# Optimization experiments

Hardware: AMD Instinct MI355X
Metric: run time of the kernel (lower is better)

Reference implementation:

```python
import jax, jax.numpy as jnp
import numpy as np

B, S, HID = 2, 2048, 2048
N_HEADS, N_KV = 16, 4
HEAD_DIM = HID // N_HEADS  # 128
N_REP = N_HEADS // N_KV
ROPE_THETA = 1000000.0


def setup_inputs() -> dict:
    key = jax.random.key(0)
    ks = jax.random.split(key, 8)
    s = 0.02
    # causal additive mask: 0 on/below diagonal, large negative above
    neg = jnp.finfo(jnp.float32).min
    causal = jnp.where(jnp.tril(jnp.ones((S, S), dtype=bool)), 0.0, neg)
    attention_mask = jnp.broadcast_to(causal[None, None], (B, 1, S, S)).astype(jnp.float32)
    return {
        "hidden_states": jax.random.normal(ks[0], (B, S, HID), jnp.float32),
        "Wq": jax.random.normal(ks[1], (HID, HID), jnp.float32) * s,
        "bq": jax.random.normal(ks[2], (HID,), jnp.float32) * s,
        "Wk": jax.random.normal(ks[3], (N_KV * HEAD_DIM, HID), jnp.float32) * s,
        "bk": jax.random.normal(ks[4], (N_KV * HEAD_DIM,), jnp.float32) * s,
        "Wv": jax.random.normal(ks[5], (N_KV * HEAD_DIM, HID), jnp.float32) * s,
        "bv": jax.random.normal(ks[6], (N_KV * HEAD_DIM,), jnp.float32) * s,
        "attention_mask": attention_mask,
        "position_ids": jnp.broadcast_to(jnp.arange(S, dtype=jnp.int64)[None], (B, S)),
    }


def _rotate_half(x):
    x1, x2 = jnp.split(x, 2, axis=-1)
    return jnp.concatenate((-x2, x1), axis=-1)


def _rope_cos_sin(position_ids, dtype):
    inv_freq = 1.0 / (ROPE_THETA ** (jnp.arange(0, HEAD_DIM, 2, dtype=jnp.float32) / HEAD_DIM))
    freqs = position_ids.astype(jnp.float32)[:, :, None] * inv_freq[None, None, :]  # [B,S,hd/2]
    emb = jnp.concatenate((freqs, freqs), axis=-1)  # [B,S,hd]
    return jnp.cos(emb).astype(dtype), jnp.sin(emb).astype(dtype)


def reference(hidden_states, Wq, bq, Wk, bk, Wv, bv, attention_mask, position_ids):
    b, s, _ = hidden_states.shape
    q = (hidden_states @ Wq.T + bq).reshape(b, s, N_HEADS, HEAD_DIM).transpose(0, 2, 1, 3)
    k = (hidden_states @ Wk.T + bk).reshape(b, s, N_KV, HEAD_DIM).transpose(0, 2, 1, 3)
    v = (hidden_states @ Wv.T + bv).reshape(b, s, N_KV, HEAD_DIM).transpose(0, 2, 1, 3)

    cos, sin = _rope_cos_sin(position_ids, hidden_states.dtype)
    cos, sin = cos[:, None], sin[:, None]  # unsqueeze head dim
    q = q * cos + _rotate_half(q) * sin
    k = k * cos + _rotate_half(k) * sin

    # GQA: repeat kv heads
    k = jnp.repeat(k, N_REP, axis=1)
    v = jnp.repeat(v, N_REP, axis=1)

    scores = jnp.einsum('bhqd,bhkd->bhqk', q, k) / jnp.sqrt(jnp.float32(HEAD_DIM)).astype(q.dtype)
    scores = scores + attention_mask
    probs = jax.nn.softmax(scores.astype(jnp.float32), axis=-1).astype(q.dtype)
    out = jnp.einsum('bhqk,bhkd->bhqd', probs, v)  # [B,H,S,hd]
    return out.transpose(0, 2, 1, 3).reshape(b, s, HID)
```

## Files before the change

### kernel.cpp

```cpp
#include <hip/hip_runtime.h>
#include <hip/hip_bf16.h>

typedef short bf16x8 __attribute__((ext_vector_type(8)));
typedef float f32x4 __attribute__((ext_vector_type(4)));
typedef unsigned int u32;
typedef unsigned short u16;

#define SLEN 2048
#define LOG2S 11

__device__ __forceinline__ u16 f2bf(float x) {
  u32 u = __builtin_bit_cast(u32, x);
  u = (u + 0x7fffu + ((u >> 16) & 1u)) >> 16;
  return (u16)u;
}

__device__ __forceinline__ void gload16(const void* g, void* l) {
  __builtin_amdgcn_global_load_lds((const __attribute__((address_space(1))) u32*)g,
                                   (__attribute__((address_space(3))) u32*)l, 16, 0, 0);
}

#define MFMA16(a, b, c) __builtin_amdgcn_mfma_f32_16x16x32_bf16((a), (b), (c), 0, 0, 0)

__global__ void k_convert(const float* __restrict__ src, u16* __restrict__ dst, int n4) {
  int i = blockIdx.x * blockDim.x + threadIdx.x;
  int stride = gridDim.x * blockDim.x;
  for (; i < n4; i += stride) {
    float4 v = reinterpret_cast<const float4*>(src)[i];
    ushort4 o;
    o.x = f2bf(v.x); o.y = f2bf(v.y); o.z = f2bf(v.z); o.w = f2bf(v.w);
    reinterpret_cast<ushort4*>(dst)[i] = o;
  }
}

__global__ void k_rope_table(float* __restrict__ ctab, float* __restrict__ stab) {
  int i = blockIdx.x * blockDim.x + threadIdx.x;
  int s = i >> 6, d = i & 63;
  float invf = powf(1.0e6f, -(float)d * (1.0f / 64.0f));
  float a = (float)s * invf;
  ctab[i] = cosf(a);
  stab[i] = sinf(a);
}

__global__ __launch_bounds__(256, 2) void k_proj(
    const u16* __restrict__ Xb, const u16* __restrict__ Wqb,
    const u16* __restrict__ Wkb, const u16* __restrict__ Wvb,
    const float* __restrict__ bq, const float* __restrict__ bk, const float* __restrict__ bv,
    const float* __restrict__ ctab, const float* __restrict__ stab,
    u16* __restrict__ Qb, u16* __restrict__ Kb, u16* __restrict__ Vt) {
  __shared__ __align__(16) char smb[65536];
  const int tid = threadIdx.x;
  const int lane = tid & 63;
  const int w = tid >> 6;
  const int l15 = lane & 15, g = lane >> 4;
  const int m0 = blockIdx.x * 128;
  const int y = blockIdx.y;
  int mode, head;
  const u16* W; const float* bias;
  if (y < 16)      { mode = 0; head = y;      W = Wqb; bias = bq; }
  else if (y < 20) { mode = 1; head = y - 16; W = Wkb; bias = bk; }
  else             { mode = 2; head = y - 20; W = Wvb; bias = bv; }
  const int n0 = head * 128;

  f32x4 acc[2][8] = {};

  const char* asrc[4]; const char* bsrc[4]; int ldo[4];
  #pragma unroll
  for (int it = 0; it < 4; ++it) {
    int c = it * 256 + tid;
    int row = c >> 3;
    int inner = ((c & 7) << 4) ^ ((row & 7) << 4);
    asrc[it] = (const char*)Xb + ((size_t)(m0 + row) * 2048) * 2 + inner;
    bsrc[it] = (const char*)W  + ((size_t)(n0 + row) * 2048) * 2 + inner;
    ldo[it] = c * 16;
  }

  auto STAGE = [&](int buf, int t) {
    char* ad = smb + buf * 16384;
    char* bd = smb + 32768 + buf * 16384;
    #pragma unroll
    for (int it = 0; it < 4; ++it) gload16(asrc[it] + t * 128, ad + ldo[it]);
    #pragma unroll
    for (int it = 0; it < 4; ++it) gload16(bsrc[it] + t * 128, bd + ldo[it]);
  };

  STAGE(0, 0);
  int cur = 0;
  for (int t = 0; t < 32; ++t) {
    if (t + 1 < 32) {
      STAGE(cur ^ 1, t + 1);
      asm volatile("s_waitcnt vmcnt(8)" ::: "memory");
    } else {
      asm volatile("s_waitcnt vmcnt(0)" ::: "memory");
    }
    __builtin_amdgcn_s_barrier();
    asm volatile("" ::: "memory");
    const char* Ac = smb + cur * 16384;
    const char* Bc = smb + 32768 + cur * 16384;
    #pragma unroll
    for (int kf = 0; kf < 2; ++kf) {
      const int innerk = kf * 64 + g * 16;
      const int rowA0 = w * 32 + l15;
      const int rowA1 = rowA0 + 16;
      bf16x8 a0 = *(const bf16x8*)(Ac + rowA0 * 128 + (innerk ^ ((rowA0 & 7) << 4)));
      bf16x8 a1 = *(const bf16x8*)(Ac + rowA1 * 128 + (innerk ^ ((rowA1 & 7) << 4)));
      #pragma unroll
      for (int j = 0; j < 8; ++j) {
        const int rowB = j * 16 + l15;
        bf16x8 bb = *(const bf16x8*)(Bc + rowB * 128 + (innerk ^ ((rowB & 7) << 4)));
        acc[0][j] = MFMA16(a0, bb, acc[0][j]);
        acc[1][j] = MFMA16(a1, bb, acc[1][j]);
      }
    }
    asm volatile("" ::: "memory");
    __builtin_amdgcn_s_barrier();
    cur ^= 1;
  }

  float biasv[8];
  #pragma unroll
  for (int j = 0; j < 8; ++j) biasv[j] = bias[n0 + j * 16 + l15];

  #pragma unroll
  for (int i = 0; i < 2; ++i) {
    #pragma unroll
    for (int r = 0; r < 4; ++r) {
      const int m = m0 + w * 32 + i * 16 + g * 4 + r;
      const int b = m >> LOG2S, s = m & (SLEN - 1);
      float v[8];
      #pragma unroll
      for (int j = 0; j < 8; ++j) v[j] = acc[i][j][r] + biasv[j];
      if (mode <= 1) {
        #pragma unroll
        for (int j = 0; j < 4; ++j) {
          const int f = j * 16 + l15;
          const float cv = ctab[s * 64 + f];
          const float sv = stab[s * 64 + f];
          const float lo = v[j], hi = v[j + 4];
          v[j]     = lo * cv - hi * sv;
          v[j + 4] = hi * cv + lo * sv;
        }
      }
      if (mode == 0) {
        u16* dst = Qb + (((size_t)(b * 16 + head) * SLEN + s) * 128);
        #pragma unroll
        for (int j = 0; j < 8; ++j) dst[j * 16 + l15] = f2bf(v[j]);
      } else if (mode == 1) {
        u16* dst = Kb + (((size_t)(b * 4 + head) * SLEN + s) * 128);
        #pragma unroll
        for (int j = 0; j < 8; ++j) dst[j * 16 + l15] = f2bf(v[j]);
      } else {
        const int sl = w * 32 + i * 16 + g * 4 + r;
        #pragma unroll
        for (int j = 0; j < 8; ++j) {
          const int d = j * 16 + l15;
          *(u16*)(smb + d * 256 + ((sl * 2) ^ ((d & 7) << 4))) = f2bf(v[j]);
        }
      }
    }
  }
  if (mode == 2) {
    __syncthreads();
    const int sbase = m0 & (SLEN - 1);
    const int bidx = m0 >> LOG2S;
    u16* Vg = Vt + ((size_t)(bidx * 4 + head) * 128) * SLEN;
    #pragma unroll
    for (int itr = 0; itr < 8; ++itr) {
      int c = itr * 256 + tid;
      int d = c >> 4, sc = c & 15;
      bf16x8 val = *(const bf16x8*)(smb + d * 256 + ((sc * 16) ^ ((d & 7) << 4)));
      *(bf16x8*)(Vg + (size_t)d * SLEN + sbase + sc * 8) = val;
    }
  }
}

__global__ __launch_bounds__(256, 2) void k_attn(
    const u16* __restrict__ Qb, const u16* __restrict__ Kb, const u16* __restrict__ Vt,
    float* __restrict__ Out) {
  __shared__ __align__(16) char smb[73728];
  const int tid = threadIdx.x, lane = tid & 63, w = tid >> 6;
  const int l15 = lane & 15, g = lane >> 4;
  const int qb_t = blockIdx.x;
  const int qa_t = 31 - qb_t;
  const int bh = blockIdx.y;
  const int b = bh >> 4, h = bh & 15, kv = h >> 2;
  const u16* Qbase = Qb + ((size_t)(b * 16 + h) * SLEN) * 128;
  const char* Kg = (const char*)(Kb + ((size_t)(b * 4 + kv) * SLEN) * 128);
  const char* Vg = (const char*)(Vt + ((size_t)(b * 4 + kv) * 128) * SLEN);
  char* Pw = smb + 65536 + w * 2048;

  const char* srcK[4]; const char* srcV[4]; int ldo[4];
  #pragma unroll
  for (int it = 0; it < 4; ++it) {
    int c = it * 256 + tid;
    ldo[it] = c * 16;
    int rk = c >> 4;
    srcK[it] = Kg + (size_t)rk * 256 + (((c & 15) << 4) ^ ((rk & 7) << 4));
    int rv = c >> 3;
    srcV[it] = Vg + (size_t)rv * 4096 + (((c & 7) << 4) ^ ((rv & 7) << 4));
  }

  const int qwa = qa_t * 64 + w * 16, qwb = qb_t * 64 + w * 16;
  bf16x8 qfa[4], qfb[4];
  #pragma unroll
  for (int kf = 0; kf < 4; ++kf) {
    qfa[kf] = *(const bf16x8*)(Qbase + (size_t)(qwa + l15) * 128 + kf * 32 + g * 8);
    qfb[kf] = *(const bf16x8*)(Qbase + (size_t)(qwb + l15) * 128 + kf * 32 + g * 8);
  }

  float ma[4], la[4], mb[4], lb[4];
  f32x4 oa[8] = {}, ob[8] = {};
  #pragma unroll
  for (int r = 0; r < 4; ++r) { ma[r] = mb[r] = -1e30f; la[r] = lb[r] = 0.f; }
  const float scale = 0.08838834764831845f;
  const int nt = qa_t + 1;

  auto STAGE = [&](int buf, int t) {
    char* kd = smb + buf * 16384;
    char* vd = smb + 32768 + buf * 16384;
    size_t ko = (size_t)t * 64;
    #pragma unroll
    for (int it = 0; it < 4; ++it) gload16(srcK[it] + ko * 256, kd + ldo[it]);
    #pragma unroll
    for (int it = 0; it < 4; ++it) gload16(srcV[it] + ko * 2, vd + ldo[it]);
  };

  STAGE(0, 0);
  int cur = 0;
  for (int t = 0; t < nt; ++t) {
    if (t + 1 < nt) {
      STAGE(cur ^ 1, t + 1);
      asm volatile("s_waitcnt vmcnt(8)" ::: "memory");
    } else {
      asm volatile("s_waitcnt vmcnt(0)" ::: "memory");
    }
    __builtin_amdgcn_s_barrier();
    asm volatile("" ::: "memory");
    const char* Kc = smb + cur * 16384;
    const char* Vc = smb + 32768 + cur * 16384;
    const int k0 = t * 64;

    auto softmax_pv = [&](f32x4* sac, float* mrun, float* lrun, f32x4* oacc,
                          int qw, bool diag) {
      float pr[4][4], alpha[4];
      #pragma unroll
      for (int r = 0; r < 4; ++r) {
        float sv[4];
        #pragma unroll
        for (int n = 0; n < 4; ++n) {
          float x = sac[n][r] * scale;
          if (diag) {
            int kvi = k0 + n * 16 + l15;
            int qi = qw + g * 4 + r;
            if (kvi > qi) x = -1e30f;
          }
          sv[n] = x;
        }
        float tm = fmaxf(fmaxf(sv[0], sv[1]), fmaxf(sv[2], sv[3]));
        tm = fmaxf(tm, __shfl_xor(tm, 1));
        tm = fmaxf(tm, __shfl_xor(tm, 2));
        tm = fmaxf(tm, __shfl_xor(tm, 4));
        tm = fmaxf(tm, __shfl_xor(tm, 8));
        float mnew = fmaxf(mrun[r], tm);
        alpha[r] = __expf(mrun[r] - mnew);
        mrun[r] = mnew;
        float ts = 0.f;
        #pragma unroll
        for (int n = 0; n < 4; ++n) { pr[n][r] = __expf(sv[n] - mnew); ts += pr[n][r]; }
        ts += __shfl_xor(ts, 1);
        ts += __shfl_xor(ts, 2);
        ts += __shfl_xor(ts, 4);
        ts += __shfl_xor(ts, 8);
        lrun[r] = lrun[r] * alpha[r] + ts;
      }
      #pragma unroll
      for (int nf = 0; nf < 8; ++nf) {
        #pragma unroll
        for (int r = 0; r < 4; ++r) oacc[nf][r] *= alpha[r];
      }
      #pragma unroll
      for (int n = 0; n < 4; ++n) {
        #pragma unroll
        for (int r = 0; r < 4; ++r) {
          const int row = g * 4 + r;
          const int colb = ((n * 16 + l15) * 2) ^ ((row & 7) << 4);
          *(u16*)(Pw + row * 128 + colb) = f2bf(pr[n][r]);
        }
      }
      #pragma unroll
      for (int kf2 = 0; kf2 < 2; ++kf2) {
        const int innerk = kf2 * 64 + g * 16;
        bf16x8 pa = *(const bf16x8*)(Pw + l15 * 128 + (innerk ^ ((l15 & 7) << 4)));
        #pragma unroll
        for (int nf = 0; nf < 8; ++nf) {
          const int row = nf * 16 + l15;
          bf16x8 vb = *(const bf16x8*)(Vc + row * 128 + (innerk ^ ((row & 7) << 4)));
          oacc[nf] = MFMA16(pa, vb, oacc[nf]);
        }
      }
    };

    auto tilebody = [&](bool dob) {
      f32x4 sa4[4] = {}, sb4[4] = {};
      #pragma unroll
      for (int kf = 0; kf < 4; ++kf) {
        const int innerk = kf * 64 + g * 16;
        #pragma unroll
        for (int n = 0; n < 4; ++n) {
          const int row = n * 16 + l15;
          bf16x8 kb = *(const bf16x8*)(Kc + row * 256 + (innerk ^ ((row & 7) << 4)));
          sa4[n] = MFMA16(qfa[kf], kb, sa4[n]);
          if (dob) sb4[n] = MFMA16(qfb[kf], kb, sb4[n]);
        }
      }
      softmax_pv(sa4, ma, la, oa, qwa, t == qa_t);
      if (dob) softmax_pv(sb4, mb, lb, ob, qwb, t == qb_t);
    };
    if (t <= qb_t) tilebody(true); else tilebody(false);

    asm volatile("" ::: "memory");
    __builtin_amdgcn_s_barrier();
    cur ^= 1;
  }

  #pragma unroll
  for (int r = 0; r < 4; ++r) {
    const float inv = 1.0f / la[r];
    const int q = qwa + g * 4 + r;
    float* dst = Out + ((size_t)(b * SLEN + q) * 2048) + h * 128;
    #pragma unroll
    for (int nf = 0; nf < 8; ++nf) dst[nf * 16 + l15] = oa[nf][r] * inv;
  }
  #pragma unroll
  for (int r = 0; r < 4; ++r) {
    const float inv = 1.0f / lb[r];
    const int q = qwb + g * 4 + r;
    float* dst = Out + ((size_t)(b * SLEN + q) * 2048) + h * 128;
    #pragma unroll
    for (int nf = 0; nf < 8; ++nf) dst[nf * 16 + l15] = ob[nf][r] * inv;
  }
}

extern "C" void kernel_launch(void* const* d_in, const int* in_sizes, int n_in,
                              void* d_out, int out_size, void* d_ws, size_t ws_size,
                              hipStream_t stream) {
  const float* X  = (const float*)d_in[0];
  const float* Wq = (const float*)d_in[1];
  const float* bq = (const float*)d_in[2];
  const float* Wk = (const float*)d_in[3];
  const float* bk = (const float*)d_in[4];
  const float* Wv = (const float*)d_in[5];
  const float* bv = (const float*)d_in[6];
  float* Out = (float*)d_out;
  char* ws = (char*)d_ws;
  u16* Xb    = (u16*)(ws + 0);
  u16* Wqb   = (u16*)(ws + 16777216);
  u16* Wkb   = (u16*)(ws + 25165824);
  u16* Wvb   = (u16*)(ws + 27262976);
  u16* Qb    = (u16*)(ws + 29360128);
  u16* Kb    = (u16*)(ws + 46137344);
  u16* Vt    = (u16*)(ws + 50331648);
  float* ctab = (float*)(ws + 54525952);
  float* stab = (float*)(ws + 55050240);

  hipLaunchKernelGGL(k_convert, dim3(2048), dim3(256), 0, stream, X,  Xb,  2097152);
  hipLaunchKernelGGL(k_convert, dim3(1024), dim3(256), 0, stream, Wq, Wqb, 1048576);
  hipLaunchKernelGGL(k_convert, dim3(512),  dim3(256), 0, stream, Wk, Wkb, 262144);
  hipLaunchKernelGGL(k_convert, dim3(512),  dim3(256), 0, stream, Wv, Wvb, 262144);
  hipLaunchKernelGGL(k_rope_table, dim3(512), dim3(256), 0, stream, ctab, stab);
  hipLaunchKernelGGL(k_proj, dim3(32, 24), dim3(256), 0, stream,
                     Xb, Wqb, Wkb, Wvb, bq, bk, bv, ctab, stab, Qb, Kb, Vt);
  hipLaunchKernelGGL(k_attn, dim3(16, 32), dim3(256), 0, stream, Qb, Kb, Vt, Out);
}
```

Measured before the change: 324.9 us.

## Rework attention kernel with smaller KV tiles, transposed scores, lazy rescale, fused conversions

The four fp32-to-bf16 conversion launches are merged into one kernel, and the softmax scale is folded into the Q projection epilogue. The attention kernel now uses 32-row KV tiles with 48KB of LDS, which allows 3 blocks per CU. It computes transposed S tiles so each lane owns one query row, skips the rescale of the running max unless the max grows by more than 8, packs P writes, and skips tiles that are fully masked per wave. Block IDs are remapped to spread work, but the smaller tiles double barrier and loop overhead per unit of work.

```diff
diff --git a/kernel.cpp b/kernel.cpp
--- a/kernel.cpp
+++ b/kernel.cpp
@@ -15,6 +15,10 @@
   return (u16)u;
 }
 
+__device__ __forceinline__ u32 pkbf(float a, float b) {
+  return (u32)f2bf(a) | ((u32)f2bf(b) << 16);
+}
+
 __device__ __forceinline__ void gload16(const void* g, void* l) {
   __builtin_amdgcn_global_load_lds((const __attribute__((address_space(1))) u32*)g,
                                    (__attribute__((address_space(3))) u32*)l, 16, 0, 0);
@@ -22,14 +26,24 @@
 
 #define MFMA16(a, b, c) __builtin_amdgcn_mfma_f32_16x16x32_bf16((a), (b), (c), 0, 0, 0)
 
-__global__ void k_convert(const float* __restrict__ src, u16* __restrict__ dst, int n4) {
+__global__ void k_convert4(const float* __restrict__ s0, u16* __restrict__ d0,
+                           const float* __restrict__ s1, u16* __restrict__ d1,
+                           const float* __restrict__ s2, u16* __restrict__ d2,
+                           const float* __restrict__ s3, u16* __restrict__ d3) {
+  const int n0 = 2097152, n1 = 1048576, n2 = 262144, n3 = 262144;
+  const int total = n0 + n1 + n2 + n3;
   int i = blockIdx.x * blockDim.x + threadIdx.x;
   int stride = gridDim.x * blockDim.x;
-  for (; i < n4; i += stride) {
-    float4 v = reinterpret_cast<const float4*>(src)[i];
+  for (; i < total; i += stride) {
+    const float* s; u16* d; int j = i;
+    if (j < n0) { s = s0; d = d0; }
+    else if ((j -= n0) < n1) { s = s1; d = d1; }
+    else if ((j -= n1) < n2) { s = s2; d = d2; }
+    else { j -= n2; s = s3; d = d3; }
+    float4 v = reinterpret_cast<const float4*>(s)[j];
     ushort4 o;
     o.x = f2bf(v.x); o.y = f2bf(v.y); o.z = f2bf(v.z); o.w = f2bf(v.w);
-    reinterpret_cast<ushort4*>(dst)[i] = o;
+    reinterpret_cast<ushort4*>(d)[j] = o;
   }
 }
 
@@ -142,6 +156,8 @@
         }
       }
       if (mode == 0) {
+        #pragma unroll
+        for (int j = 0; j < 8; ++j) v[j] *= 0.08838834764831845f;
         u16* dst = Qb + (((size_t)(b * 16 + head) * SLEN + s) * 128);
         #pragma unroll
         for (int j = 0; j < 8; ++j) dst[j * 16 + l15] = f2bf(v[j]);
@@ -174,30 +190,33 @@
   }
 }
 
-__global__ __launch_bounds__(256, 2) void k_attn(
+__global__ __launch_bounds__(256, 3) void k_attn(
     const u16* __restrict__ Qb, const u16* __restrict__ Kb, const u16* __restrict__ Vt,
     float* __restrict__ Out) {
-  __shared__ __align__(16) char smb[73728];
+  __shared__ __align__(16) char smb[49152];
   const int tid = threadIdx.x, lane = tid & 63, w = tid >> 6;
   const int l15 = lane & 15, g = lane >> 4;
-  const int qb_t = blockIdx.x;
+  const int lid = blockIdx.y * 16 + blockIdx.x;
+  const int sl = lid >> 3;
+  const int bh = (lid & 7) * 4 + (sl & 3);
+  const int qb_t = sl >> 2;
   const int qa_t = 31 - qb_t;
-  const int bh = blockIdx.y;
   const int b = bh >> 4, h = bh & 15, kv = h >> 2;
   const u16* Qbase = Qb + ((size_t)(b * 16 + h) * SLEN) * 128;
   const char* Kg = (const char*)(Kb + ((size_t)(b * 4 + kv) * SLEN) * 128);
   const char* Vg = (const char*)(Vt + ((size_t)(b * 4 + kv) * 128) * SLEN);
-  char* Pw = smb + 65536 + w * 2048;
-
-  const char* srcK[4]; const char* srcV[4]; int ldo[4];
-  #pragma unroll
-  for (int it = 0; it < 4; ++it) {
+  char* Pwa = smb + 32768 + w * 4096;
+  char* Pwb = Pwa + 2048;
+
+  const char* srcK[2]; const char* srcV[2]; int ldoK[2], ldoV[2];
+  #pragma unroll
+  for (int it = 0; it < 2; ++it) {
     int c = it * 256 + tid;
-    ldo[it] = c * 16;
+    ldoK[it] = c * 16; ldoV[it] = c * 16;
     int rk = c >> 4;
     srcK[it] = Kg + (size_t)rk * 256 + (((c & 15) << 4) ^ ((rk & 7) << 4));
-    int rv = c >> 3;
-    srcV[it] = Vg + (size_t)rv * 4096 + (((c & 7) << 4) ^ ((rv & 7) << 4));
+    int rv = c >> 2;
+    srcV[it] = Vg + (size_t)rv * (SLEN * 2) + (((c & 3) << 4) ^ (((rv >> 1) & 3) << 4));
   }
 
   const int qwa = qa_t * 64 + w * 16, qwb = qb_t * 64 + w * 16;
@@ -208,21 +227,63 @@
     qfb[kf] = *(const bf16x8*)(Qbase + (size_t)(qwb + l15) * 128 + kf * 32 + g * 8);
   }
 
-  float ma[4], la[4], mb[4], lb[4];
+  float ma = -1e30f, la = 0.f, mb = -1e30f, lb = 0.f;
   f32x4 oa[8] = {}, ob[8] = {};
-  #pragma unroll
-  for (int r = 0; r < 4; ++r) { ma[r] = mb[r] = -1e30f; la[r] = lb[r] = 0.f; }
-  const float scale = 0.08838834764831845f;
-  const int nt = qa_t + 1;
+  const int nt = 2 * qa_t + 2;
 
   auto STAGE = [&](int buf, int t) {
-    char* kd = smb + buf * 16384;
-    char* vd = smb + 32768 + buf * 16384;
-    size_t ko = (size_t)t * 64;
-    #pragma unroll
-    for (int it = 0; it < 4; ++it) gload16(srcK[it] + ko * 256, kd + ldo[it]);
-    #pragma unroll
-    for (int it = 0; it < 4; ++it) gload16(srcV[it] + ko * 2, vd + ldo[it]);
+    char* kd = smb + buf * 8192;
+    char* vd = smb + 16384 + buf * 8192;
+    const size_t koK = (size_t)t * 8192;
+    const size_t koV = (size_t)t * 64;
+    #pragma unroll
+    for (int it = 0; it < 2; ++it) gload16(srcK[it] + koK, kd + ldoK[it]);
+    #pragma unroll
+    for (int it = 0; it < 2; ++it) gload16(srcV[it] + koV, vd + ldoV[it]);
+  };
+
+  auto softmax = [&](f32x4* sc, float& m, float& l, f32x4* oacc, char* Pdst,
+                     int k0, int qw, bool maskneed) {
+    float sv[8];
+    #pragma unroll
+    for (int n = 0; n < 2; ++n) {
+      #pragma unroll
+      for (int r = 0; r < 4; ++r) {
+        float x = sc[n][r];
+        if (maskneed && (k0 + n * 16 + g * 4 + r > qw + l15)) x = -1e30f;
+        sv[n * 4 + r] = x;
+      }
+    }
+    float tm = fmaxf(fmaxf(fmaxf(sv[0], sv[1]), fmaxf(sv[2], sv[3])),
+                     fmaxf(fmaxf(sv[4], sv[5]), fmaxf(sv[6], sv[7])));
+    tm = fmaxf(tm, __shfl_xor(tm, 16));
+    tm = fmaxf(tm, __shfl_xor(tm, 32));
+    if (__any(tm > m + 8.0f)) {
+      float mnew = fmaxf(m, tm);
+      float alpha = __expf(m - mnew);
+      m = mnew;
+      l *= alpha;
+      #pragma unroll
+      for (int r = 0; r < 4; ++r) {
+        float ar = __shfl(alpha, g * 4 + r);
+        #pragma unroll
+        for (int nf = 0; nf < 8; ++nf) oacc[nf][r] *= ar;
+      }
+    }
+    float p[8];
+    #pragma unroll
+    for (int i2 = 0; i2 < 8; ++i2) p[i2] = __expf(sv[i2] - m);
+    float ts = ((p[0] + p[1]) + (p[2] + p[3])) + ((p[4] + p[5]) + (p[6] + p[7]));
+    ts += __shfl_xor(ts, 16);
+    ts += __shfl_xor(ts, 32);
+    l += ts;
+    #pragma unroll
+    for (int n = 0; n < 2; ++n) {
+      uint2 pk;
+      pk.x = pkbf(p[n * 4 + 0], p[n * 4 + 1]);
+      pk.y = pkbf(p[n * 4 + 2], p[n * 4 + 3]);
+      *(uint2*)(Pdst + l15 * 128 + ((n * 32 + g * 8) ^ ((l15 & 7) << 4))) = pk;
+    }
   };
 
   STAGE(0, 0);
@@ -230,102 +291,53 @@
   for (int t = 0; t < nt; ++t) {
     if (t + 1 < nt) {
       STAGE(cur ^ 1, t + 1);
-      asm volatile("s_waitcnt vmcnt(8)" ::: "memory");
+      asm volatile("s_waitcnt vmcnt(4)" ::: "memory");
     } else {
       asm volatile("s_waitcnt vmcnt(0)" ::: "memory");
     }
     __builtin_amdgcn_s_barrier();
     asm volatile("" ::: "memory");
-    const char* Kc = smb + cur * 16384;
-    const char* Vc = smb + 32768 + cur * 16384;
-    const int k0 = t * 64;
-
-    auto softmax_pv = [&](f32x4* sac, float* mrun, float* lrun, f32x4* oacc,
-                          int qw, bool diag) {
-      float pr[4][4], alpha[4];
-      #pragma unroll
-      for (int r = 0; r < 4; ++r) {
-        float sv[4];
-        #pragma unroll
-        for (int n = 0; n < 4; ++n) {
-          float x = sac[n][r] * scale;
-          if (diag) {
-            int kvi = k0 + n * 16 + l15;
-            int qi = qw + g * 4 + r;
-            if (kvi > qi) x = -1e30f;
-          }
-          sv[n] = x;
+    const char* Kc = smb + cur * 8192;
+    const char* Vc = smb + 16384 + cur * 8192;
+    const int k0 = t * 32;
+    const bool act_a = (k0 <= qwa + 15);
+    const bool act_b = (t < 2 * qb_t + 2) && (k0 <= qwb + 15);
+
+    if (act_a | act_b) {
+      f32x4 sa[2] = {}, sb[2] = {};
+      #pragma unroll
+      for (int kf = 0; kf < 4; ++kf) {
+        #pragma unroll
+        for (int n = 0; n < 2; ++n) {
+          const int row = n * 16 + l15;
+          bf16x8 kb = *(const bf16x8*)(Kc + row * 256 + ((kf * 64 + g * 16) ^ ((row & 7) << 4)));
+          if (act_a) sa[n] = MFMA16(kb, qfa[kf], sa[n]);
+          if (act_b) sb[n] = MFMA16(kb, qfb[kf], sb[n]);
         }
-        float tm = fmaxf(fmaxf(sv[0], sv[1]), fmaxf(sv[2], sv[3]));
-        tm = fmaxf(tm, __shfl_xor(tm, 1));
-        tm = fmaxf(tm, __shfl_xor(tm, 2));
-        tm = fmaxf(tm, __shfl_xor(tm, 4));
-        tm = fmaxf(tm, __shfl_xor(tm, 8));
-        float mnew = fmaxf(mrun[r], tm);
-        alpha[r] = __expf(mrun[r] - mnew);
-        mrun[r] = mnew;
-        float ts = 0.f;
-        #pragma unroll
-        for (int n = 0; n < 4; ++n) { pr[n][r] = __expf(sv[n] - mnew); ts += pr[n][r]; }
-        ts += __shfl_xor(ts, 1);
-        ts += __shfl_xor(ts, 2);
-        ts += __shfl_xor(ts, 4);
-        ts += __shfl_xor(ts, 8);
-        lrun[r] = lrun[r] * alpha[r] + ts;
-      }
+      }
+      if (act_a) softmax(sa, ma, la, oa, Pwa, k0, qwa, k0 + 31 > qwa);
+      if (act_b) softmax(sb, mb, lb, ob, Pwb, k0, qwb, k0 + 31 > qwb);
+
+      bf16x8 paa = {}, pab = {};
+      if (act_a) paa = *(const bf16x8*)(Pwa + l15 * 128 + ((g * 16) ^ ((l15 & 7) << 4)));
+      if (act_b) pab = *(const bf16x8*)(Pwb + l15 * 128 + ((g * 16) ^ ((l15 & 7) << 4)));
       #pragma unroll
       for (int nf = 0; nf < 8; ++nf) {
-        #pragma unroll
-        for (int r = 0; r < 4; ++r) oacc[nf][r] *= alpha[r];
-      }
-      #pragma unroll
-      for (int n = 0; n < 4; ++n) {
-        #pragma unroll
-        for (int r = 0; r < 4; ++r) {
-          const int row = g * 4 + r;
-          const int colb = ((n * 16 + l15) * 2) ^ ((row & 7) << 4);
-          *(u16*)(Pw + row * 128 + colb) = f2bf(pr[n][r]);
-        }
-      }
-      #pragma unroll
-      for (int kf2 = 0; kf2 < 2; ++kf2) {
-        const int innerk = kf2 * 64 + g * 16;
-        bf16x8 pa = *(const bf16x8*)(Pw + l15 * 128 + (innerk ^ ((l15 & 7) << 4)));
-        #pragma unroll
-        for (int nf = 0; nf < 8; ++nf) {
-          const int row = nf * 16 + l15;
-          bf16x8 vb = *(const bf16x8*)(Vc + row * 128 + (innerk ^ ((row & 7) << 4)));
-          oacc[nf] = MFMA16(pa, vb, oacc[nf]);
-        }
-      }
-    };
-
-    auto tilebody = [&](bool dob) {
-      f32x4 sa4[4] = {}, sb4[4] = {};
-      #pragma unroll
-      for (int kf = 0; kf < 4; ++kf) {
-        const int innerk = kf * 64 + g * 16;
-        #pragma unroll
-        for (int n = 0; n < 4; ++n) {
-          const int row = n * 16 + l15;
-          bf16x8 kb = *(const bf16x8*)(Kc + row * 256 + (innerk ^ ((row & 7) << 4)));
-          sa4[n] = MFMA16(qfa[kf], kb, sa4[n]);
-          if (dob) sb4[n] = MFMA16(qfb[kf], kb, sb4[n]);
-        }
-      }
-      softmax_pv(sa4, ma, la, oa, qwa, t == qa_t);
-      if (dob) softmax_pv(sb4, mb, lb, ob, qwb, t == qb_t);
-    };
-    if (t <= qb_t) tilebody(true); else tilebody(false);
-
+        const int row = nf * 16 + l15;
+        bf16x8 vb = *(const bf16x8*)(Vc + row * 64 + ((g * 16) ^ (((row >> 1) & 3) << 4)));
+        if (act_a) oa[nf] = MFMA16(paa, vb, oa[nf]);
+        if (act_b) ob[nf] = MFMA16(pab, vb, ob[nf]);
+      }
+    }
     asm volatile("" ::: "memory");
     __builtin_amdgcn_s_barrier();
     cur ^= 1;
   }
 
+  float lia = 1.0f / la, lib = 1.0f / lb;
   #pragma unroll
   for (int r = 0; r < 4; ++r) {
-    const float inv = 1.0f / la[r];
+    float inv = __shfl(lia, g * 4 + r);
     const int q = qwa + g * 4 + r;
     float* dst = Out + ((size_t)(b * SLEN + q) * 2048) + h * 128;
     #pragma unroll
@@ -333,7 +345,7 @@
   }
   #pragma unroll
   for (int r = 0; r < 4; ++r) {
-    const float inv = 1.0f / lb[r];
+    float inv = __shfl(lib, g * 4 + r);
     const int q = qwb + g * 4 + r;
     float* dst = Out + ((size_t)(b * SLEN + q) * 2048) + h * 128;
     #pragma unroll
@@ -363,10 +375,8 @@
   float* ctab = (float*)(ws + 54525952);
   float* stab = (float*)(ws + 55050240);
 
-  hipLaunchKernelGGL(k_convert, dim3(2048), dim3(256), 0, stream, X,  Xb,  2097152);
-  hipLaunchKernelGGL(k_convert, dim3(1024), dim3(256), 0, stream, Wq, Wqb, 1048576);
-  hipLaunchKernelGGL(k_convert, dim3(512),  dim3(256), 0, stream, Wk, Wkb, 262144);
-  hipLaunchKernelGGL(k_convert, dim3(512),  dim3(256), 0, stream, Wv, Wvb, 262144);
+  hipLaunchKernelGGL(k_convert4, dim3(2048), dim3(256), 0, stream,
+                     X, Xb, Wq, Wqb, Wk, Wkb, Wv, Wvb);
   hipLaunchKernelGGL(k_rope_table, dim3(512), dim3(256), 0, stream, ctab, stab);
   hipLaunchKernelGGL(k_proj, dim3(32, 24), dim3(256), 0, stream,
                      Xb, Wqb, Wkb, Wvb, bq, bk, bv, ctab, stab, Qb, Kb, Vt);
```

New measurement: 291.3 us. -10.4%, faster.
